# Performance work log

Measured on AMD Instinct MI355X. Metric: run time of the kernel, lower is better.

The kernel has to match this reference:

```python
import jax, jax.numpy as jnp
import numpy as np

B, SX, SY, D = 64, 512, 512, 1024


def setup_inputs() -> dict:
    key = jax.random.key(0)
    k1, k2, k3, k4 = jax.random.split(key, 4)
    x = jax.random.normal(k1, (B, SX, D), dtype=jnp.float32)
    y = jax.random.normal(k2, (B, SY, D), dtype=jnp.float32)
    # Keras 'uniform' init ~ U(-0.05, 0.05); scale kept small and realistic
    W = jax.random.uniform(k3, (D, D), dtype=jnp.float32, minval=-0.05, maxval=0.05)
    b = jax.random.uniform(k4, (D,), dtype=jnp.float32, minval=-0.05, maxval=0.05)
    return {"x": x, "y": y, "W": W, "b": b}


def reference(x, y, W, b):
    # proj: (x @ W + b) -> [B, Sx, D]
    proj = jnp.einsum('bsd,de->bse', x, W) + b
    # attention scores: proj @ y^T -> [B, Sx, Sy]
    att = jnp.einsum('bsd,btd->bst', proj, y)
    # row-wise stable softmax over last axis (matches manual max-subtract softmax)
    nor = jax.nn.softmax(att, axis=-1)
    # weighted sum over y -> [B, Sx, D]
    return jnp.einsum('bst,btd->bsd', nor, y)
```

## Files before the change

### kernel.cpp

```cpp
#include <hip/hip_runtime.h>


typedef float  f32x4  __attribute__((ext_vector_type(4)));
typedef _Float16 f16x8 __attribute__((ext_vector_type(8)));
typedef _Float16 f16x4 __attribute__((ext_vector_type(4)));
typedef __bf16 bf16x8 __attribute__((ext_vector_type(8)));
typedef __bf16 bf16x4 __attribute__((ext_vector_type(4)));

#define MFMA_F16(a, b, c)  __builtin_amdgcn_mfma_f32_16x16x32_f16((a), (b), (c), 0, 0, 0)
#define MFMA_BF16(a, b, c) __builtin_amdgcn_mfma_f32_16x16x32_bf16((a), (b), (c), 0, 0, 0)

#define WAIT_VM0()  do { asm volatile("s_waitcnt vmcnt(0)" ::: "memory"); \
                         __builtin_amdgcn_sched_barrier(0); } while (0)
#define WAIT_LGKM0() do { asm volatile("s_waitcnt lgkmcnt(0)" ::: "memory"); \
                          __builtin_amdgcn_sched_barrier(0); } while (0)

__device__ __forceinline__ void async16(const void* g, void* lds) {
    __builtin_amdgcn_global_load_lds(
        (const __attribute__((address_space(1))) unsigned int*)g,
        (__attribute__((address_space(3))) unsigned int*)lds, 16, 0, 0);
}


__global__ void prep_y_kernel(const float* __restrict__ y, _Float16* __restrict__ yf,
                              _Float16* __restrict__ yT)
{
    __shared__ _Float16 LT[64][72];
    const int tid = threadIdx.x;
    const int b   = blockIdx.x >> 7;
    const int rem = blockIdx.x & 127;
    const int sy0 = (rem >> 4) * 64;
    const int d0  = (rem & 15) * 64;
    const int r0 = tid >> 4;
    const int c4 = (tid & 15) * 4;
    #pragma unroll
    for (int i = 0; i < 4; ++i) {
        const int r = r0 + i * 16;
        const float4 v = *(const float4*)&y[((size_t)b * 512 + sy0 + r) * 1024 + d0 + c4];
        const f16x4 hv = {(_Float16)v.x, (_Float16)v.y, (_Float16)v.z, (_Float16)v.w};
        *(f16x4*)&yf[((size_t)b * 512 + sy0 + r) * 1024 + d0 + c4] = hv;
        #pragma unroll
        for (int cc = 0; cc < 4; ++cc) {
            const int c = (cc + (tid & 3)) & 3;
            LT[c4 + c][r] = hv[c];
        }
    }
    __syncthreads();
    #pragma unroll
    for (int i = 0; i < 4; ++i) {
        const int dr = r0 + i * 16;
        const f16x4 v = *(const f16x4*)&LT[dr][(tid & 15) * 4];
        *(f16x4*)&yT[((size_t)b * 1024 + d0 + dr) * 512 + sy0 + (tid & 15) * 4] = v;
    }
}

__global__ void prep_w_kernel(const float* __restrict__ W, _Float16* __restrict__ WT)
{
    __shared__ _Float16 LT[64][72];
    const int tid = threadIdx.x;
    const int k0 = (blockIdx.x >> 4) * 64;
    const int n0 = (blockIdx.x & 15) * 64;
    const int r0 = tid >> 4;
    const int c4 = (tid & 15) * 4;
    #pragma unroll
    for (int i = 0; i < 4; ++i) {
        const int r = r0 + i * 16;
        const float4 v = *(const float4*)&W[(size_t)(k0 + r) * 1024 + n0 + c4];
        const f16x4 hv = {(_Float16)v.x, (_Float16)v.y, (_Float16)v.z, (_Float16)v.w};
        #pragma unroll
        for (int cc = 0; cc < 4; ++cc) {
            const int c = (cc + (tid & 3)) & 3;
            LT[c4 + c][r] = hv[c];
        }
    }
    __syncthreads();
    #pragma unroll
    for (int i = 0; i < 4; ++i) {
        const int dr = r0 + i * 16;
        const f16x4 v = *(const f16x4*)&LT[dr][(tid & 15) * 4];
        *(f16x4*)&WT[(size_t)(n0 + dr) * 1024 + k0 + (tid & 15) * 4] = v;
    }
}

__global__ void cvt_hl_kernel(const float4* __restrict__ in, f16x4* __restrict__ oh,
                              f16x4* __restrict__ ol, int n4)
{
    int i = blockIdx.x * blockDim.x + threadIdx.x;
    const int stride = gridDim.x * blockDim.x;
    for (; i < n4; i += stride) {
        const float4 v = in[i];
        const _Float16 h0 = (_Float16)v.x, h1 = (_Float16)v.y,
                       h2 = (_Float16)v.z, h3 = (_Float16)v.w;
        oh[i] = (f16x4){h0, h1, h2, h3};
        ol[i] = (f16x4){(_Float16)(v.x - (float)h0), (_Float16)(v.y - (float)h1),
                        (_Float16)(v.z - (float)h2), (_Float16)(v.w - (float)h3)};
    }
}

template <bool PRE>
__global__ __launch_bounds__(256, 3)
void proj_f16_kernel(const _Float16* __restrict__ xh, const _Float16* __restrict__ xl,
                     const _Float16* __restrict__ WT, const float* __restrict__ W,
                     const float* __restrict__ bias, char* __restrict__ outc)
{
    __shared__ _Float16 Xh[128][32];
    __shared__ _Float16 Xl[128][32];
    __shared__ _Float16 Wf[128][32];

    const int tid = threadIdx.x, lane = tid & 63, wave = tid >> 6;
    const int swz = (blockIdx.x & 7) * 256 + (blockIdx.x >> 3);
    const int m0 = (swz >> 3) * 128, n0 = (swz & 7) * 128;
    const int wm = (wave >> 1) * 64, wn = (wave & 1) * 64;
    const int ar = lane & 15;
    const int qs  = ((lane >> 4) ^ ((lane >> 1) & 3)) * 8;
    const int gcS = ((lane & 3) ^ ((lane >> 3) & 3)) * 8;

    f32x4 acc[4][4];
    #pragma unroll
    for (int i = 0; i < 4; ++i)
        #pragma unroll
        for (int j = 0; j < 4; ++j)
            acc[i][j] = (f32x4){0.f, 0.f, 0.f, 0.f};

    const int lrow = lane >> 2;
    const int wkb = tid & 7;
    const int wn4 = (tid >> 3) * 4;

    for (int k0 = 0; k0 < 1024; k0 += 32) {
        __syncthreads();
        #pragma unroll
        for (int t = 0; t < 2; ++t) {
            const int r = wave * 32 + t * 16 + lrow;
            async16(&xh[(size_t)(m0 + r) * 1024 + k0 + gcS], &Xh[wave * 32 + t * 16][0]);
            async16(&xl[(size_t)(m0 + r) * 1024 + k0 + gcS], &Xl[wave * 32 + t * 16][0]);
            if constexpr (PRE)
                async16(&WT[(size_t)(n0 + r) * 1024 + k0 + gcS], &Wf[wave * 32 + t * 16][0]);
        }
        if constexpr (!PRE) {
            const size_t wb = (size_t)(k0 + wkb * 4) * 1024 + n0 + wn4;
            const float4 v0 = *(const float4*)&W[wb];
            const float4 v1 = *(const float4*)&W[wb + 1024];
            const float4 v2 = *(const float4*)&W[wb + 2048];
            const float4 v3 = *(const float4*)&W[wb + 3072];
            const float rv[4][4] = {{v0.x, v0.y, v0.z, v0.w},
                                    {v1.x, v1.y, v1.z, v1.w},
                                    {v2.x, v2.y, v2.z, v2.w},
                                    {v3.x, v3.y, v3.z, v3.w}};
            #pragma unroll
            for (int j = 0; j < 4; ++j) {
                const int R = wn4 + j;
                const f16x4 hv = {(_Float16)rv[0][j], (_Float16)rv[1][j],
                                  (_Float16)rv[2][j], (_Float16)rv[3][j]};
                const int c = (wkb >> 1) ^ ((R >> 1) & 3);
                *(f16x4*)&Wf[R][c * 8 + (wkb & 1) * 4] = hv;
            }
        }
        __syncthreads();

        f16x8 ah[4], al[4], bf[4];
        #pragma unroll
        for (int f = 0; f < 4; ++f) {
            ah[f] = *(const f16x8*)&Xh[wm + f * 16 + ar][qs];
            al[f] = *(const f16x8*)&Xl[wm + f * 16 + ar][qs];
            bf[f] = *(const f16x8*)&Wf[wn + f * 16 + ar][qs];
        }
        #pragma unroll
        for (int i = 0; i < 4; ++i)
            #pragma unroll
            for (int j = 0; j < 4; ++j) {
                acc[i][j] = MFMA_F16(ah[i], bf[j], acc[i][j]);
                acc[i][j] = MFMA_F16(al[i], bf[j], acc[i][j]);
            }
    }

    const int q4 = (lane >> 4) * 4;
    #pragma unroll
    for (int j = 0; j < 4; ++j) {
        const int n = n0 + wn + j * 16 + ar;
        const float bv = bias[n];
        #pragma unroll
        for (int i = 0; i < 4; ++i)
            #pragma unroll
            for (int r = 0; r < 4; ++r) {
                const int R = m0 + wm + i * 16 + q4 + r;
                const float v = acc[i][j][r] + bv;
                const _Float16 h = (_Float16)v;
                const _Float16 l = (_Float16)(v - (float)h);
                _Float16* rowp = (_Float16*)(outc + (size_t)R * 4096);
                rowp[n] = h;
                rowp[1024 + n] = l;
            }
    }
}

__global__ __launch_bounds__(256, 2)
void attn_f16_kernel(const _Float16* __restrict__ yf, const _Float16* __restrict__ yT,
                     char* __restrict__ outc)
{
    __shared__ __align__(16) char smem[76800];
    _Float16 (*Yst)[32]   = (_Float16(*)[32])smem;
    _Float16 (*Pbuf)[520] = (_Float16(*)[520])smem;
    _Float16 (*Yt)[32]    = (_Float16(*)[32])(smem + 66560);
    float*    Red         = (float*)(smem + 74752);

    const int tid = threadIdx.x, lane = tid & 63, wave = tid >> 6;
    const int swz = (blockIdx.x & 7) * 64 + (blockIdx.x >> 3);
    const int b = swz >> 3, sx0 = (swz & 7) * 64;
    const int pbase = b * 512 + sx0;
    const int ar = lane & 15, q = lane >> 4, qk = q * 8;
    const int qs  = (q ^ ((lane >> 1) & 3)) * 8;
    const int gcS = ((lane & 3) ^ ((lane >> 3) & 3)) * 8;
    const int lrow = lane >> 2;
    const size_t ybase = (size_t)b * 512 * 1024;

    f32x4 s2[4][8];
    #pragma unroll
    for (int ri = 0; ri < 4; ++ri)
        #pragma unroll
        for (int t = 0; t < 8; ++t)
            s2[ri][t] = (f32x4){0.f, 0.f, 0.f, 0.f};

    const char* aptr = outc + (size_t)(pbase + ar) * 4096;

    #pragma unroll
    for (int t = 0; t < 8; ++t) {
        const int r = wave * 128 + t * 16 + lrow;
        async16(&yf[ybase + (size_t)r * 1024 + gcS], &Yst[wave * 128 + t * 16][0]);
    }
    f16x8 aH[4], aL[4];
    #pragma unroll
    for (int ri = 0; ri < 4; ++ri) {
        aH[ri] = *(const f16x8*)(aptr + (size_t)ri * 65536 + (size_t)qk * 2);
        aL[ri] = *(const f16x8*)(aptr + (size_t)ri * 65536 + 2048 + (size_t)qk * 2);
    }

    for (int kk = 0; kk < 32; ++kk) {
        WAIT_VM0();
        f16x8 bf0[8];
        #pragma unroll
        for (int t = 0; t < 8; ++t)
            bf0[t] = *(const f16x8*)&Yst[wave * 128 + t * 16 + ar][qs];
        WAIT_LGKM0();
        if (kk < 31) {
            const int k1 = (kk + 1) * 32;
            #pragma unroll
            for (int t = 0; t < 8; ++t) {
                const int r = wave * 128 + t * 16 + lrow;
                async16(&yf[ybase + (size_t)r * 1024 + k1 + gcS],
                        &Yst[wave * 128 + t * 16][0]);
            }
        }
        #pragma unroll
        for (int ri = 0; ri < 4; ++ri)
            #pragma unroll
            for (int t = 0; t < 8; ++t) {
                s2[ri][t] = MFMA_F16(aH[ri], bf0[t], s2[ri][t]);
                s2[ri][t] = MFMA_F16(aL[ri], bf0[t], s2[ri][t]);
            }
        if (kk < 31) {
            const int k1 = (kk + 1) * 32;
            #pragma unroll
            for (int ri = 0; ri < 4; ++ri) {
                aH[ri] = *(const f16x8*)(aptr + (size_t)ri * 65536 + (size_t)(k1 + qk) * 2);
                aL[ri] = *(const f16x8*)(aptr + (size_t)ri * 65536 + 2048
                                         + (size_t)(k1 + qk) * 2);
            }
        }
    }

    float pm[4][4];
    #pragma unroll
    for (int ri = 0; ri < 4; ++ri)
        #pragma unroll
        for (int r = 0; r < 4; ++r) {
            float m = -3.0e38f;
            #pragma unroll
            for (int t = 0; t < 8; ++t) m = fmaxf(m, s2[ri][t][r]);
            pm[ri][r] = m;
        }
    #pragma unroll
    for (int off = 1; off < 16; off <<= 1)
        #pragma unroll
        for (int ri = 0; ri < 4; ++ri)
            #pragma unroll
            for (int r = 0; r < 4; ++r)
                pm[ri][r] = fmaxf(pm[ri][r], __shfl_xor(pm[ri][r], off, 64));
    if (ar == 0) {
        #pragma unroll
        for (int ri = 0; ri < 4; ++ri)
            #pragma unroll
            for (int r = 0; r < 4; ++r)
                Red[wave * 64 + ri * 16 + q * 4 + r] = pm[ri][r];
    }
    __syncthreads();
    float gm[4][4];
    #pragma unroll
    for (int ri = 0; ri < 4; ++ri)
        #pragma unroll
        for (int r = 0; r < 4; ++r) {
            const int row = ri * 16 + q * 4 + r;
            gm[ri][r] = fmaxf(fmaxf(Red[row], Red[64 + row]),
                              fmaxf(Red[128 + row], Red[192 + row]));
        }
    float ps[4][4];
    #pragma unroll
    for (int ri = 0; ri < 4; ++ri)
        #pragma unroll
        for (int r = 0; r < 4; ++r) {
            float sum = 0.f;
            #pragma unroll
            for (int t = 0; t < 8; ++t) {
                const float e = __expf(s2[ri][t][r] - gm[ri][r]);
                s2[ri][t][r] = e;
                sum += e;
            }
            ps[ri][r] = sum;
        }
    #pragma unroll
    for (int off = 1; off < 16; off <<= 1)
        #pragma unroll
        for (int ri = 0; ri < 4; ++ri)
            #pragma unroll
            for (int r = 0; r < 4; ++r)
                ps[ri][r] += __shfl_xor(ps[ri][r], off, 64);
    if (ar == 0) {
        #pragma unroll
        for (int ri = 0; ri < 4; ++ri)
            #pragma unroll
            for (int r = 0; r < 4; ++r)
                Red[256 + wave * 64 + ri * 16 + q * 4 + r] = ps[ri][r];
    }
    __syncthreads();
    float inv[4][4];
    #pragma unroll
    for (int ri = 0; ri < 4; ++ri)
        #pragma unroll
        for (int r = 0; r < 4; ++r) {
            const int row = 256 + ri * 16 + q * 4 + r;
            inv[ri][r] = 1.0f / (Red[row] + Red[64 + row] + Red[128 + row] + Red[192 + row]);
        }
    #pragma unroll
    for (int ri = 0; ri < 4; ++ri)
        #pragma unroll
        for (int t = 0; t < 8; ++t)
            #pragma unroll
            for (int r = 0; r < 4; ++r)
                Pbuf[ri * 16 + q * 4 + r][wave * 128 + t * 16 + ar]
                    = (_Float16)(s2[ri][t][r] * inv[ri][r]);
    __syncthreads();

    float* outF = (float*)outc;
    for (int dc = 0; dc < 8; ++dc) {
        f32x4 o2[4][2];
        #pragma unroll
        for (int ri = 0; ri < 4; ++ri)
            #pragma unroll
            for (int t = 0; t < 2; ++t)
                o2[ri][t] = (f32x4){0.f, 0.f, 0.f, 0.f};

        WAIT_LGKM0();
        #pragma unroll
        for (int t = 0; t < 2; ++t) {
            const int r = wave * 32 + t * 16 + lrow;
            async16(&yT[(size_t)(b * 1024 + dc * 128 + r) * 512 + gcS],
                    &Yt[wave * 32 + t * 16][0]);
        }
        for (int kk = 0; kk < 16; ++kk) {
            WAIT_VM0();
            f16x8 a2[4], b2[2];
            #pragma unroll
            for (int ri = 0; ri < 4; ++ri)
                a2[ri] = *(const f16x8*)&Pbuf[ri * 16 + ar][kk * 32 + qk];
            #pragma unroll
            for (int t = 0; t < 2; ++t)
                b2[t] = *(const f16x8*)&Yt[wave * 32 + t * 16 + ar][qs];
            WAIT_LGKM0();
            if (kk < 15) {
                const int k1 = (kk + 1) * 32;
                #pragma unroll
                for (int t = 0; t < 2; ++t) {
                    const int r = wave * 32 + t * 16 + lrow;
                    async16(&yT[(size_t)(b * 1024 + dc * 128 + r) * 512 + k1 + gcS],
                            &Yt[wave * 32 + t * 16][0]);
                }
            }
            #pragma unroll
            for (int ri = 0; ri < 4; ++ri)
                #pragma unroll
                for (int t = 0; t < 2; ++t)
                    o2[ri][t] = MFMA_F16(a2[ri], b2[t], o2[ri][t]);
        }
        #pragma unroll
        for (int ri = 0; ri < 4; ++ri)
            #pragma unroll
            for (int t = 0; t < 2; ++t)
                #pragma unroll
                for (int r = 0; r < 4; ++r)
                    outF[(size_t)(pbase + ri * 16 + q * 4 + r) * 1024
                         + dc * 128 + wave * 32 + t * 16 + ar] = o2[ri][t][r];
    }
}


__device__ __forceinline__ void cvt4(const float4 v, bf16x4& h, bf16x4& l) {
    const float f0 = v.x, f1 = v.y, f2 = v.z, f3 = v.w;
    const __bf16 h0 = (__bf16)f0, h1 = (__bf16)f1, h2 = (__bf16)f2, h3 = (__bf16)f3;
    h = (bf16x4){h0, h1, h2, h3};
    l = (bf16x4){(__bf16)(f0 - (float)h0), (__bf16)(f1 - (float)h1),
                 (__bf16)(f2 - (float)h2), (__bf16)(f3 - (float)h3)};
}

__global__ __launch_bounds__(256, 2)
void proj_kernel_fb(const float* __restrict__ x, const float* __restrict__ W,
                    const float* __restrict__ bias, float* __restrict__ proj)
{
    __shared__ __bf16 Ah[128][40];
    __shared__ __bf16 Al[128][40];
    __shared__ __bf16 Bh[128][40];
    __shared__ __bf16 Bl[128][40];

    const int tid = threadIdx.x, lane = tid & 63, wave = tid >> 6;
    const int wm = (wave >> 1) * 64, wn = (wave & 1) * 64;
    const int m0 = (blockIdx.x >> 3) * 128, n0 = (blockIdx.x & 7) * 128;
    const int ar = lane & 15, ak = (lane >> 4) * 8;

    f32x4 acc[4][4];
    #pragma unroll
    for (int i = 0; i < 4; ++i)
        #pragma unroll
        for (int j = 0; j < 4; ++j)
            acc[i][j] = (f32x4){0.f, 0.f, 0.f, 0.f};

    const int xr = tid >> 3, xc = (tid & 7) * 4;
    const int wkb = tid >> 5, wn4 = (tid & 31) * 4;

    for (int k0 = 0; k0 < 1024; k0 += 32) {
        __syncthreads();
        #pragma unroll
        for (int it = 0; it < 4; ++it) {
            const int r = xr + it * 32;
            const float4 v = *(const float4*)&x[(size_t)(m0 + r) * 1024 + k0 + xc];
            bf16x4 h, l; cvt4(v, h, l);
            *(bf16x4*)&Ah[r][xc] = h;
            *(bf16x4*)&Al[r][xc] = l;
        }
        {
            const size_t wb = (size_t)(k0 + wkb * 4) * 1024 + n0 + wn4;
            const float4 v0 = *(const float4*)&W[wb];
            const float4 v1 = *(const float4*)&W[wb + 1024];
            const float4 v2 = *(const float4*)&W[wb + 2048];
            const float4 v3 = *(const float4*)&W[wb + 3072];
            const float rv[4][4] = {{v0.x, v0.y, v0.z, v0.w},
                                    {v1.x, v1.y, v1.z, v1.w},
                                    {v2.x, v2.y, v2.z, v2.w},
                                    {v3.x, v3.y, v3.z, v3.w}};
            #pragma unroll
            for (int j = 0; j < 4; ++j) {
                bf16x4 h, l;
                #pragma unroll
                for (int kk = 0; kk < 4; ++kk) {
                    const float f = rv[kk][j];
                    const __bf16 hb = (__bf16)f;
                    h[kk] = hb;
                    l[kk] = (__bf16)(f - (float)hb);
                }
                *(bf16x4*)&Bh[wn4 + j][wkb * 4] = h;
                *(bf16x4*)&Bl[wn4 + j][wkb * 4] = l;
            }
        }
        __syncthreads();

        bf16x8 a_h[4], a_l[4], b_h[4], b_l[4];
        #pragma unroll
        for (int f = 0; f < 4; ++f) {
            a_h[f] = *(const bf16x8*)&Ah[wm + f * 16 + ar][ak];
            a_l[f] = *(const bf16x8*)&Al[wm + f * 16 + ar][ak];
            b_h[f] = *(const bf16x8*)&Bh[wn + f * 16 + ar][ak];
            b_l[f] = *(const bf16x8*)&Bl[wn + f * 16 + ar][ak];
        }
        #pragma unroll
        for (int i = 0; i < 4; ++i)
            #pragma unroll
            for (int j = 0; j < 4; ++j) {
                acc[i][j] = MFMA_BF16(a_h[i], b_h[j], acc[i][j]);
                acc[i][j] = MFMA_BF16(a_l[i], b_h[j], acc[i][j]);
                acc[i][j] = MFMA_BF16(a_h[i], b_l[j], acc[i][j]);
            }
    }

    const int q4 = (lane >> 4) * 4;
    #pragma unroll
    for (int j = 0; j < 4; ++j) {
        const int n = n0 + wn + j * 16 + ar;
        const float bv = bias[n];
        #pragma unroll
        for (int i = 0; i < 4; ++i) {
            const size_t base = (size_t)(m0 + wm + i * 16 + q4) * 1024 + n;
            #pragma unroll
            for (int r = 0; r < 4; ++r)
                proj[base + (size_t)r * 1024] = acc[i][j][r] + bv;
        }
    }
}

__global__ __launch_bounds__(256, 1)
void attn_kernel_fb(const float* __restrict__ y, float* __restrict__ out)
{
    __shared__ __bf16 Ph[64][40];
    __shared__ __bf16 Pl[64][40];
    __shared__ __bf16 Yh[128][40];
    __shared__ __bf16 Yl[128][40];
    __shared__ __bf16 Pbuf[64][520];

    const int tid = threadIdx.x, lane = tid & 63, wave = tid >> 6;
    const int b = blockIdx.x >> 3, sx0 = (blockIdx.x & 7) * 64;
    const size_t ybase = (size_t)b * 512 * 1024;
    const size_t pbase = ((size_t)b * 512 + sx0) * 1024;
    const int ar = lane & 15, ak = (lane >> 4) * 8, q = lane >> 4;

    f32x4 s[4][8];
    #pragma unroll
    for (int nb = 0; nb < 4; ++nb)
        #pragma unroll
        for (int f = 0; f < 8; ++f)
            s[nb][f] = (f32x4){0.f, 0.f, 0.f, 0.f};

    const int pr = tid >> 3, pc = (tid & 7) * 4;

    for (int k0 = 0; k0 < 1024; k0 += 32) {
        __syncthreads();
        #pragma unroll
        for (int it = 0; it < 2; ++it) {
            const int r = pr + it * 32;
            const float4 v = *(const float4*)&out[pbase + (size_t)r * 1024 + k0 + pc];
            bf16x4 h, l; cvt4(v, h, l);
            *(bf16x4*)&Ph[r][pc] = h;
            *(bf16x4*)&Pl[r][pc] = l;
        }
        #pragma unroll
        for (int nb = 0; nb < 4; ++nb) {
            if (nb) __syncthreads();
            const int sy0 = nb * 128;
            #pragma unroll
            for (int it = 0; it < 4; ++it) {
                const int r = pr + it * 32;
                const float4 v = *(const float4*)&y[ybase + (size_t)(sy0 + r) * 1024 + k0 + pc];
                bf16x4 h, l; cvt4(v, h, l);
                *(bf16x4*)&Yh[r][pc] = h;
                *(bf16x4*)&Yl[r][pc] = l;
            }
            __syncthreads();
            const bf16x8 a_h = *(const bf16x8*)&Ph[wave * 16 + ar][ak];
            const bf16x8 a_l = *(const bf16x8*)&Pl[wave * 16 + ar][ak];
            #pragma unroll
            for (int f = 0; f < 8; ++f) {
                const bf16x8 b_h = *(const bf16x8*)&Yh[f * 16 + ar][ak];
                const bf16x8 b_l = *(const bf16x8*)&Yl[f * 16 + ar][ak];
                s[nb][f] = MFMA_BF16(a_h, b_h, s[nb][f]);
                s[nb][f] = MFMA_BF16(a_l, b_h, s[nb][f]);
                s[nb][f] = MFMA_BF16(a_h, b_l, s[nb][f]);
            }
        }
    }

    #pragma unroll
    for (int r = 0; r < 4; ++r) {
        float m = -3.0e38f;
        #pragma unroll
        for (int nb = 0; nb < 4; ++nb)
            #pragma unroll
            for (int f = 0; f < 8; ++f)
                m = fmaxf(m, s[nb][f][r]);
        #pragma unroll
        for (int off = 1; off < 16; off <<= 1)
            m = fmaxf(m, __shfl_xor(m, off, 64));
        float sum = 0.f;
        #pragma unroll
        for (int nb = 0; nb < 4; ++nb)
            #pragma unroll
            for (int f = 0; f < 8; ++f) {
                const float e = __expf(s[nb][f][r] - m);
                s[nb][f][r] = e;
                sum += e;
            }
        #pragma unroll
        for (int off = 1; off < 16; off <<= 1)
            sum += __shfl_xor(sum, off, 64);
        const float inv = 1.0f / sum;
        #pragma unroll
        for (int nb = 0; nb < 4; ++nb)
            #pragma unroll
            for (int f = 0; f < 8; ++f)
                s[nb][f][r] *= inv;
    }
    #pragma unroll
    for (int nb = 0; nb < 4; ++nb)
        #pragma unroll
        for (int f = 0; f < 8; ++f)
            #pragma unroll
            for (int r = 0; r < 4; ++r)
                Pbuf[wave * 16 + q * 4 + r][nb * 128 + f * 16 + ar] = (__bf16)s[nb][f][r];

    const int y2kb = tid >> 5, y2n4 = (tid & 31) * 4;
    for (int d0 = 0; d0 < 1024; d0 += 128) {
        f32x4 o[8];
        #pragma unroll
        for (int f = 0; f < 8; ++f) o[f] = (f32x4){0.f, 0.f, 0.f, 0.f};

        for (int k0 = 0; k0 < 512; k0 += 32) {
            __syncthreads();
            const size_t yb = ybase + (size_t)(k0 + y2kb * 4) * 1024 + d0 + y2n4;
            const float4 v0 = *(const float4*)&y[yb];
            const float4 v1 = *(const float4*)&y[yb + 1024];
            const float4 v2 = *(const float4*)&y[yb + 2048];
            const float4 v3 = *(const float4*)&y[yb + 3072];
            const float rv[4][4] = {{v0.x, v0.y, v0.z, v0.w},
                                    {v1.x, v1.y, v1.z, v1.w},
                                    {v2.x, v2.y, v2.z, v2.w},
                                    {v3.x, v3.y, v3.z, v3.w}};
            #pragma unroll
            for (int j = 0; j < 4; ++j) {
                const bf16x4 h = (bf16x4){(__bf16)rv[0][j], (__bf16)rv[1][j],
                                          (__bf16)rv[2][j], (__bf16)rv[3][j]};
                *(bf16x4*)&Yh[y2n4 + j][y2kb * 4] = h;
            }
            __syncthreads();
            const bf16x8 a = *(const bf16x8*)&Pbuf[wave * 16 + ar][k0 + ak];
            #pragma unroll
            for (int f = 0; f < 8; ++f) {
                const bf16x8 bb = *(const bf16x8*)&Yh[f * 16 + ar][ak];
                o[f] = MFMA_BF16(a, bb, o[f]);
            }
        }
        #pragma unroll
        for (int f = 0; f < 8; ++f)
            #pragma unroll
            for (int r = 0; r < 4; ++r)
                out[pbase + (size_t)(wave * 16 + q * 4 + r) * 1024 + d0 + f * 16 + ar] = o[f][r];
    }
}


extern "C" void kernel_launch(void* const* d_in, const int* in_sizes, int n_in,
                              void* d_out, int out_size, void* d_ws, size_t ws_size,
                              hipStream_t stream) {
    (void)in_sizes; (void)n_in; (void)out_size;
    const float* x    = (const float*)d_in[0];
    const float* y    = (const float*)d_in[1];
    const float* W    = (const float*)d_in[2];
    const float* bias = (const float*)d_in[3];

    if (ws_size >= 268435456ULL) {
        _Float16* yf = (_Float16*)d_ws;
        _Float16* yT = yf + 33554432;
        _Float16* xh = yT + 33554432;
        _Float16* xl = xh + 33554432;
        _Float16* WT = xl + 33554432;
        const bool pre = ws_size >= 268435456ULL + 2097152ULL;

        prep_y_kernel<<<dim3(8192), dim3(256), 0, stream>>>(y, yf, yT);
        cvt_hl_kernel<<<dim3(2048), dim3(256), 0, stream>>>((const float4*)x, (f16x4*)xh,
                                                            (f16x4*)xl, 8388608);
        if (pre) {
            prep_w_kernel<<<dim3(256), dim3(256), 0, stream>>>(W, WT);
            proj_f16_kernel<true><<<dim3(2048), dim3(256), 0, stream>>>(xh, xl, WT, W, bias,
                                                                        (char*)d_out);
        } else {
            proj_f16_kernel<false><<<dim3(2048), dim3(256), 0, stream>>>(xh, xl, nullptr, W,
                                                                         bias, (char*)d_out);
        }
        attn_f16_kernel<<<dim3(512), dim3(256), 0, stream>>>(yf, yT, (char*)d_out);
    } else {
        float* out = (float*)d_out;
        proj_kernel_fb<<<dim3(256 * 8), dim3(256), 0, stream>>>(x, W, bias, out);
        attn_kernel_fb<<<dim3(64 * 8), dim3(256), 0, stream>>>(y, out);
    }
}
```

Before: 703.4 us.

## Double-buffer proj and attention loads, interleave proj hi/lo layout, swizzle P buffer

The projection GEMM gets double-buffered LDS stages with one barrier per k-step instead of two. The proj output's hi/lo halves are interleaved in 8-element groups so the attention kernel can read both from one contiguous 32-byte chunk. The attention kernel prefetches A fragments two steps ahead into registers, splits the Y staging into halves so loads overlap MFMA, and uses partial vmcnt waits. The softmax P buffer gets an XOR-swizzled layout and the second GEMM uses two rotating Yt buffers with a prefetch distance of two. Together these target load latency and LDS bank conflicts, at the cost of higher register and LDS pressure (AH/AL arrays and 80KB smem) that could reduce occupancy.

```diff
diff --git a/kernel.cpp b/kernel.cpp
--- a/kernel.cpp
+++ b/kernel.cpp
@@ -10,10 +10,11 @@
 #define MFMA_F16(a, b, c)  __builtin_amdgcn_mfma_f32_16x16x32_f16((a), (b), (c), 0, 0, 0)
 #define MFMA_BF16(a, b, c) __builtin_amdgcn_mfma_f32_16x16x32_bf16((a), (b), (c), 0, 0, 0)
 
-#define WAIT_VM0()  do { asm volatile("s_waitcnt vmcnt(0)" ::: "memory"); \
+#define WAIT_VM(N)  do { asm volatile("s_waitcnt vmcnt(" #N ")" ::: "memory"); \
                          __builtin_amdgcn_sched_barrier(0); } while (0)
 #define WAIT_LGKM0() do { asm volatile("s_waitcnt lgkmcnt(0)" ::: "memory"); \
                           __builtin_amdgcn_sched_barrier(0); } while (0)
+#define SB0() __builtin_amdgcn_sched_barrier(0)
 
 __device__ __forceinline__ void async16(const void* g, void* lds) {
     __builtin_amdgcn_global_load_lds(
@@ -103,9 +104,9 @@
                      const _Float16* __restrict__ WT, const float* __restrict__ W,
                      const float* __restrict__ bias, char* __restrict__ outc)
 {
-    __shared__ _Float16 Xh[128][32];
-    __shared__ _Float16 Xl[128][32];
-    __shared__ _Float16 Wf[128][32];
+    __shared__ _Float16 Xh[2][128][32];
+    __shared__ _Float16 Xl[2][128][32];
+    __shared__ _Float16 Wf[2][128][32];
 
     const int tid = threadIdx.x, lane = tid & 63, wave = tid >> 6;
     const int swz = (blockIdx.x & 7) * 256 + (blockIdx.x >> 3);
@@ -114,27 +115,26 @@
     const int ar = lane & 15;
     const int qs  = ((lane >> 4) ^ ((lane >> 1) & 3)) * 8;
     const int gcS = ((lane & 3) ^ ((lane >> 3) & 3)) * 8;
-
-    f32x4 acc[4][4];
-    #pragma unroll
-    for (int i = 0; i < 4; ++i)
-        #pragma unroll
-        for (int j = 0; j < 4; ++j)
-            acc[i][j] = (f32x4){0.f, 0.f, 0.f, 0.f};
-
     const int lrow = lane >> 2;
     const int wkb = tid & 7;
     const int wn4 = (tid >> 3) * 4;
 
-    for (int k0 = 0; k0 < 1024; k0 += 32) {
-        __syncthreads();
-        #pragma unroll
-        for (int t = 0; t < 2; ++t) {
-            const int r = wave * 32 + t * 16 + lrow;
-            async16(&xh[(size_t)(m0 + r) * 1024 + k0 + gcS], &Xh[wave * 32 + t * 16][0]);
-            async16(&xl[(size_t)(m0 + r) * 1024 + k0 + gcS], &Xl[wave * 32 + t * 16][0]);
+    f32x4 acc[4][4];
+    #pragma unroll
+    for (int i = 0; i < 4; ++i)
+        #pragma unroll
+        for (int j = 0; j < 4; ++j)
+            acc[i][j] = (f32x4){0.f, 0.f, 0.f, 0.f};
+
+    auto STAGE = [&](int t, int bi) {
+        const int k0 = t * 32;
+        #pragma unroll
+        for (int tt = 0; tt < 2; ++tt) {
+            const int r = wave * 32 + tt * 16 + lrow;
+            async16(&xh[(size_t)(m0 + r) * 1024 + k0 + gcS], &Xh[bi][wave * 32 + tt * 16][0]);
+            async16(&xl[(size_t)(m0 + r) * 1024 + k0 + gcS], &Xl[bi][wave * 32 + tt * 16][0]);
             if constexpr (PRE)
-                async16(&WT[(size_t)(n0 + r) * 1024 + k0 + gcS], &Wf[wave * 32 + t * 16][0]);
+                async16(&WT[(size_t)(n0 + r) * 1024 + k0 + gcS], &Wf[bi][wave * 32 + tt * 16][0]);
         }
         if constexpr (!PRE) {
             const size_t wb = (size_t)(k0 + wkb * 4) * 1024 + n0 + wn4;
@@ -152,17 +152,23 @@
                 const f16x4 hv = {(_Float16)rv[0][j], (_Float16)rv[1][j],
                                   (_Float16)rv[2][j], (_Float16)rv[3][j]};
                 const int c = (wkb >> 1) ^ ((R >> 1) & 3);
-                *(f16x4*)&Wf[R][c * 8 + (wkb & 1) * 4] = hv;
-            }
-        }
-        __syncthreads();
-
+                *(f16x4*)&Wf[bi][R][c * 8 + (wkb & 1) * 4] = hv;
+            }
+        }
+    };
+
+    STAGE(0, 0);
+    __syncthreads();
+
+    for (int t = 0; t < 32; ++t) {
+        const int cur = t & 1;
+        if (t < 31) STAGE(t + 1, cur ^ 1);
         f16x8 ah[4], al[4], bf[4];
         #pragma unroll
         for (int f = 0; f < 4; ++f) {
-            ah[f] = *(const f16x8*)&Xh[wm + f * 16 + ar][qs];
-            al[f] = *(const f16x8*)&Xl[wm + f * 16 + ar][qs];
-            bf[f] = *(const f16x8*)&Wf[wn + f * 16 + ar][qs];
+            ah[f] = *(const f16x8*)&Xh[cur][wm + f * 16 + ar][qs];
+            al[f] = *(const f16x8*)&Xl[cur][wm + f * 16 + ar][qs];
+            bf[f] = *(const f16x8*)&Wf[cur][wn + f * 16 + ar][qs];
         }
         #pragma unroll
         for (int i = 0; i < 4; ++i)
@@ -171,6 +177,7 @@
                 acc[i][j] = MFMA_F16(ah[i], bf[j], acc[i][j]);
                 acc[i][j] = MFMA_F16(al[i], bf[j], acc[i][j]);
             }
+        __syncthreads();
     }
 
     const int q4 = (lane >> 4) * 4;
@@ -178,6 +185,7 @@
     for (int j = 0; j < 4; ++j) {
         const int n = n0 + wn + j * 16 + ar;
         const float bv = bias[n];
+        const int hidx = (n >> 3) * 16 + (n & 7);
         #pragma unroll
         for (int i = 0; i < 4; ++i)
             #pragma unroll
@@ -187,8 +195,8 @@
                 const _Float16 h = (_Float16)v;
                 const _Float16 l = (_Float16)(v - (float)h);
                 _Float16* rowp = (_Float16*)(outc + (size_t)R * 4096);
-                rowp[n] = h;
-                rowp[1024 + n] = l;
+                rowp[hidx] = h;
+                rowp[hidx + 8] = l;
             }
     }
 }
@@ -197,17 +205,18 @@
 void attn_f16_kernel(const _Float16* __restrict__ yf, const _Float16* __restrict__ yT,
                      char* __restrict__ outc)
 {
-    __shared__ __align__(16) char smem[76800];
-    _Float16 (*Yst)[32]   = (_Float16(*)[32])smem;
-    _Float16 (*Pbuf)[520] = (_Float16(*)[520])smem;
-    _Float16 (*Yt)[32]    = (_Float16(*)[32])(smem + 66560);
-    float*    Red         = (float*)(smem + 74752);
+    __shared__ __align__(16) char smem[81920];
+    _Float16 (*Yst)[32] = (_Float16(*)[32])smem;
+    _Float16* Pb        = (_Float16*)smem;
+    _Float16 (*Yt0)[32] = (_Float16(*)[32])(smem + 65536);
+    _Float16 (*Yt1)[32] = (_Float16(*)[32])(smem + 73728);
+    float*    Red       = (float*)(smem + 73728);
 
     const int tid = threadIdx.x, lane = tid & 63, wave = tid >> 6;
-    const int swz = (blockIdx.x & 7) * 64 + (blockIdx.x >> 3);
-    const int b = swz >> 3, sx0 = (swz & 7) * 64;
+    const int swzb = (blockIdx.x & 7) * 64 + (blockIdx.x >> 3);
+    const int b = swzb >> 3, sx0 = (swzb & 7) * 64;
     const int pbase = b * 512 + sx0;
-    const int ar = lane & 15, q = lane >> 4, qk = q * 8;
+    const int ar = lane & 15, q = lane >> 4;
     const int qs  = (q ^ ((lane >> 1) & 3)) * 8;
     const int gcS = ((lane & 3) ^ ((lane >> 3) & 3)) * 8;
     const int lrow = lane >> 2;
@@ -222,50 +231,73 @@
 
     const char* aptr = outc + (size_t)(pbase + ar) * 4096;
 
+    f16x8 AH[34][4], AL[34][4];
+
     #pragma unroll
     for (int t = 0; t < 8; ++t) {
         const int r = wave * 128 + t * 16 + lrow;
         async16(&yf[ybase + (size_t)r * 1024 + gcS], &Yst[wave * 128 + t * 16][0]);
     }
-    f16x8 aH[4], aL[4];
-    #pragma unroll
-    for (int ri = 0; ri < 4; ++ri) {
-        aH[ri] = *(const f16x8*)(aptr + (size_t)ri * 65536 + (size_t)qk * 2);
-        aL[ri] = *(const f16x8*)(aptr + (size_t)ri * 65536 + 2048 + (size_t)qk * 2);
-    }
-
+    #pragma unroll
+    for (int kk = 0; kk < 2; ++kk)
+        #pragma unroll
+        for (int ri = 0; ri < 4; ++ri) {
+            AH[kk][ri] = *(const f16x8*)(aptr + (size_t)ri * 65536 + (kk * 4 + q) * 32);
+            AL[kk][ri] = *(const f16x8*)(aptr + (size_t)ri * 65536 + (kk * 4 + q) * 32 + 16);
+        }
+
+    #pragma unroll
     for (int kk = 0; kk < 32; ++kk) {
-        WAIT_VM0();
-        f16x8 bf0[8];
-        #pragma unroll
-        for (int t = 0; t < 8; ++t)
-            bf0[t] = *(const f16x8*)&Yst[wave * 128 + t * 16 + ar][qs];
+        if (kk < 31) { WAIT_VM(8); } else { WAIT_VM(0); }
+        f16x8 bfA[4];
+        #pragma unroll
+        for (int t = 0; t < 4; ++t)
+            bfA[t] = *(const f16x8*)&Yst[wave * 128 + t * 16 + ar][qs];
         WAIT_LGKM0();
         if (kk < 31) {
             const int k1 = (kk + 1) * 32;
             #pragma unroll
-            for (int t = 0; t < 8; ++t) {
+            for (int t = 0; t < 4; ++t) {
                 const int r = wave * 128 + t * 16 + lrow;
-                async16(&yf[ybase + (size_t)r * 1024 + k1 + gcS],
-                        &Yst[wave * 128 + t * 16][0]);
-            }
-        }
+                async16(&yf[ybase + (size_t)r * 1024 + k1 + gcS], &Yst[wave * 128 + t * 16][0]);
+            }
+        }
+        if (kk < 30) {
+            #pragma unroll
+            for (int ri = 0; ri < 4; ++ri) {
+                AH[kk + 2][ri] = *(const f16x8*)(aptr + (size_t)ri * 65536 + ((kk + 2) * 4 + q) * 32);
+                AL[kk + 2][ri] = *(const f16x8*)(aptr + (size_t)ri * 65536 + ((kk + 2) * 4 + q) * 32 + 16);
+            }
+        }
+        SB0();
         #pragma unroll
         for (int ri = 0; ri < 4; ++ri)
             #pragma unroll
-            for (int t = 0; t < 8; ++t) {
-                s2[ri][t] = MFMA_F16(aH[ri], bf0[t], s2[ri][t]);
-                s2[ri][t] = MFMA_F16(aL[ri], bf0[t], s2[ri][t]);
-            }
+            for (int t = 0; t < 4; ++t) {
+                s2[ri][t] = MFMA_F16(AH[kk][ri], bfA[t], s2[ri][t]);
+                s2[ri][t] = MFMA_F16(AL[kk][ri], bfA[t], s2[ri][t]);
+            }
+        f16x8 bfB[4];
+        #pragma unroll
+        for (int t = 4; t < 8; ++t)
+            bfB[t - 4] = *(const f16x8*)&Yst[wave * 128 + t * 16 + ar][qs];
+        WAIT_LGKM0();
         if (kk < 31) {
             const int k1 = (kk + 1) * 32;
             #pragma unroll
-            for (int ri = 0; ri < 4; ++ri) {
-                aH[ri] = *(const f16x8*)(aptr + (size_t)ri * 65536 + (size_t)(k1 + qk) * 2);
-                aL[ri] = *(const f16x8*)(aptr + (size_t)ri * 65536 + 2048
-                                         + (size_t)(k1 + qk) * 2);
-            }
-        }
+            for (int t = 4; t < 8; ++t) {
+                const int r = wave * 128 + t * 16 + lrow;
+                async16(&yf[ybase + (size_t)r * 1024 + k1 + gcS], &Yst[wave * 128 + t * 16][0]);
+            }
+        }
+        SB0();
+        #pragma unroll
+        for (int ri = 0; ri < 4; ++ri)
+            #pragma unroll
+            for (int t = 4; t < 8; ++t) {
+                s2[ri][t] = MFMA_F16(AH[kk][ri], bfB[t - 4], s2[ri][t]);
+                s2[ri][t] = MFMA_F16(AL[kk][ri], bfB[t - 4], s2[ri][t]);
+            }
     }
 
     float pm[4][4];
@@ -344,12 +376,28 @@
         #pragma unroll
         for (int t = 0; t < 8; ++t)
             #pragma unroll
-            for (int r = 0; r < 4; ++r)
-                Pbuf[ri * 16 + q * 4 + r][wave * 128 + t * 16 + ar]
+            for (int r = 0; r < 4; ++r) {
+                const int row = ri * 16 + q * 4 + r;
+                const int c = wave * 16 + t * 2 + (ar >> 3);
+                Pb[row * 512 + ((c ^ (row & 7)) << 3) + (ar & 7)]
                     = (_Float16)(s2[ri][t][r] * inv[ri][r]);
+            }
     __syncthreads();
 
     float* outF = (float*)outc;
+    #pragma unroll
+    for (int t = 0; t < 2; ++t) {
+        const int r = wave * 32 + t * 16 + lrow;
+        async16(&yT[(size_t)(b * 1024 + 0 * 128 + r) * 512 + 0 * 32 + gcS],
+                &Yt0[wave * 32 + t * 16][0]);
+    }
+    #pragma unroll
+    for (int t = 0; t < 2; ++t) {
+        const int r = wave * 32 + t * 16 + lrow;
+        async16(&yT[(size_t)(b * 1024 + 0 * 128 + r) * 512 + 1 * 32 + gcS],
+                &Yt1[wave * 32 + t * 16][0]);
+    }
+
     for (int dc = 0; dc < 8; ++dc) {
         f32x4 o2[4][2];
         #pragma unroll
@@ -358,32 +406,39 @@
             for (int t = 0; t < 2; ++t)
                 o2[ri][t] = (f32x4){0.f, 0.f, 0.f, 0.f};
 
-        WAIT_LGKM0();
-        #pragma unroll
-        for (int t = 0; t < 2; ++t) {
-            const int r = wave * 32 + t * 16 + lrow;
-            async16(&yT[(size_t)(b * 1024 + dc * 128 + r) * 512 + gcS],
-                    &Yt[wave * 32 + t * 16][0]);
-        }
+        #pragma unroll
         for (int kk = 0; kk < 16; ++kk) {
-            WAIT_VM0();
+            if (kk == 0) {
+                if (dc == 0) { WAIT_VM(2); } else { WAIT_VM(10); }
+            } else if (kk == 15) {
+                if (dc == 7) { WAIT_VM(0); } else { WAIT_VM(2); }
+            } else {
+                WAIT_VM(2);
+            }
+            _Float16 (*Ycur)[32] = (kk & 1) ? Yt1 : Yt0;
             f16x8 a2[4], b2[2];
             #pragma unroll
-            for (int ri = 0; ri < 4; ++ri)
-                a2[ri] = *(const f16x8*)&Pbuf[ri * 16 + ar][kk * 32 + qk];
+            for (int ri = 0; ri < 4; ++ri) {
+                const int rowa = ri * 16 + ar;
+                a2[ri] = *(const f16x8*)&Pb[rowa * 512 + (((kk * 4 + q) ^ (ar & 7)) << 3)];
+            }
             #pragma unroll
             for (int t = 0; t < 2; ++t)
-                b2[t] = *(const f16x8*)&Yt[wave * 32 + t * 16 + ar][qs];
+                b2[t] = *(const f16x8*)&Ycur[wave * 32 + t * 16 + ar][qs];
             WAIT_LGKM0();
-            if (kk < 15) {
-                const int k1 = (kk + 1) * 32;
-                #pragma unroll
-                for (int t = 0; t < 2; ++t) {
-                    const int r = wave * 32 + t * 16 + lrow;
-                    async16(&yT[(size_t)(b * 1024 + dc * 128 + r) * 512 + k1 + gcS],
-                            &Yt[wave * 32 + t * 16][0]);
+            {
+                const int kk2 = (kk + 2) & 15;
+                const int dc2 = dc + ((kk + 2) >> 4);
+                if (dc2 < 8) {
+                    #pragma unroll
+                    for (int t = 0; t < 2; ++t) {
+                        const int r = wave * 32 + t * 16 + lrow;
+                        async16(&yT[(size_t)(b * 1024 + dc2 * 128 + r) * 512 + kk2 * 32 + gcS],
+                                &Ycur[wave * 32 + t * 16][0]);
+                    }
                 }
             }
+            SB0();
             #pragma unroll
             for (int ri = 0; ri < 4; ++ri)
                 #pragma unroll
```

Result: slower. 812.5 us (+15.5%).

## Double-buffer proj GEMM, interleave hi/lo proj layout, read y directly from global in attention

Applied to the files above, without the earlier changes.

The projection GEMM now double-buffers its LDS tiles so the next K-slice loads while MFMAs run, with one barrier per iteration. Its output interleaves the fp16 hi/lo halves in 8-element groups, so the attention kernel fetches each pair with one contiguous load. The attention kernel drops LDS staging of y and yT and reads B fragments straight from global memory, keeping two A fragments in registers as a prefetch. The PV stage is restructured so each wave computes 128 output columns per pass with more accumulators, which raises register pressure and relies on caches for the repeated global reads.

```diff
diff --git a/kernel.cpp b/kernel.cpp
--- a/kernel.cpp
+++ b/kernel.cpp
@@ -9,11 +9,6 @@
 
 #define MFMA_F16(a, b, c)  __builtin_amdgcn_mfma_f32_16x16x32_f16((a), (b), (c), 0, 0, 0)
 #define MFMA_BF16(a, b, c) __builtin_amdgcn_mfma_f32_16x16x32_bf16((a), (b), (c), 0, 0, 0)
-
-#define WAIT_VM0()  do { asm volatile("s_waitcnt vmcnt(0)" ::: "memory"); \
-                         __builtin_amdgcn_sched_barrier(0); } while (0)
-#define WAIT_LGKM0() do { asm volatile("s_waitcnt lgkmcnt(0)" ::: "memory"); \
-                          __builtin_amdgcn_sched_barrier(0); } while (0)
 
 __device__ __forceinline__ void async16(const void* g, void* lds) {
     __builtin_amdgcn_global_load_lds(
@@ -103,9 +98,9 @@
                      const _Float16* __restrict__ WT, const float* __restrict__ W,
                      const float* __restrict__ bias, char* __restrict__ outc)
 {
-    __shared__ _Float16 Xh[128][32];
-    __shared__ _Float16 Xl[128][32];
-    __shared__ _Float16 Wf[128][32];
+    __shared__ _Float16 Xh[2][128][32];
+    __shared__ _Float16 Xl[2][128][32];
+    __shared__ _Float16 Wf[2][128][32];
 
     const int tid = threadIdx.x, lane = tid & 63, wave = tid >> 6;
     const int swz = (blockIdx.x & 7) * 256 + (blockIdx.x >> 3);
@@ -114,27 +109,26 @@
     const int ar = lane & 15;
     const int qs  = ((lane >> 4) ^ ((lane >> 1) & 3)) * 8;
     const int gcS = ((lane & 3) ^ ((lane >> 3) & 3)) * 8;
-
-    f32x4 acc[4][4];
-    #pragma unroll
-    for (int i = 0; i < 4; ++i)
-        #pragma unroll
-        for (int j = 0; j < 4; ++j)
-            acc[i][j] = (f32x4){0.f, 0.f, 0.f, 0.f};
-
     const int lrow = lane >> 2;
     const int wkb = tid & 7;
     const int wn4 = (tid >> 3) * 4;
 
-    for (int k0 = 0; k0 < 1024; k0 += 32) {
-        __syncthreads();
-        #pragma unroll
-        for (int t = 0; t < 2; ++t) {
-            const int r = wave * 32 + t * 16 + lrow;
-            async16(&xh[(size_t)(m0 + r) * 1024 + k0 + gcS], &Xh[wave * 32 + t * 16][0]);
-            async16(&xl[(size_t)(m0 + r) * 1024 + k0 + gcS], &Xl[wave * 32 + t * 16][0]);
+    f32x4 acc[4][4];
+    #pragma unroll
+    for (int i = 0; i < 4; ++i)
+        #pragma unroll
+        for (int j = 0; j < 4; ++j)
+            acc[i][j] = (f32x4){0.f, 0.f, 0.f, 0.f};
+
+    auto STAGE = [&](int t, int bi) {
+        const int k0 = t * 32;
+        #pragma unroll
+        for (int tt = 0; tt < 2; ++tt) {
+            const int r = wave * 32 + tt * 16 + lrow;
+            async16(&xh[(size_t)(m0 + r) * 1024 + k0 + gcS], &Xh[bi][wave * 32 + tt * 16][0]);
+            async16(&xl[(size_t)(m0 + r) * 1024 + k0 + gcS], &Xl[bi][wave * 32 + tt * 16][0]);
             if constexpr (PRE)
-                async16(&WT[(size_t)(n0 + r) * 1024 + k0 + gcS], &Wf[wave * 32 + t * 16][0]);
+                async16(&WT[(size_t)(n0 + r) * 1024 + k0 + gcS], &Wf[bi][wave * 32 + tt * 16][0]);
         }
         if constexpr (!PRE) {
             const size_t wb = (size_t)(k0 + wkb * 4) * 1024 + n0 + wn4;
@@ -152,17 +146,23 @@
                 const f16x4 hv = {(_Float16)rv[0][j], (_Float16)rv[1][j],
                                   (_Float16)rv[2][j], (_Float16)rv[3][j]};
                 const int c = (wkb >> 1) ^ ((R >> 1) & 3);
-                *(f16x4*)&Wf[R][c * 8 + (wkb & 1) * 4] = hv;
-            }
-        }
-        __syncthreads();
-
+                *(f16x4*)&Wf[bi][R][c * 8 + (wkb & 1) * 4] = hv;
+            }
+        }
+    };
+
+    STAGE(0, 0);
+    __syncthreads();
+
+    for (int t = 0; t < 32; ++t) {
+        const int cur = t & 1;
+        if (t < 31) STAGE(t + 1, cur ^ 1);
         f16x8 ah[4], al[4], bf[4];
         #pragma unroll
         for (int f = 0; f < 4; ++f) {
-            ah[f] = *(const f16x8*)&Xh[wm + f * 16 + ar][qs];
-            al[f] = *(const f16x8*)&Xl[wm + f * 16 + ar][qs];
-            bf[f] = *(const f16x8*)&Wf[wn + f * 16 + ar][qs];
+            ah[f] = *(const f16x8*)&Xh[cur][wm + f * 16 + ar][qs];
+            al[f] = *(const f16x8*)&Xl[cur][wm + f * 16 + ar][qs];
+            bf[f] = *(const f16x8*)&Wf[cur][wn + f * 16 + ar][qs];
         }
         #pragma unroll
         for (int i = 0; i < 4; ++i)
@@ -171,6 +171,7 @@
                 acc[i][j] = MFMA_F16(ah[i], bf[j], acc[i][j]);
                 acc[i][j] = MFMA_F16(al[i], bf[j], acc[i][j]);
             }
+        __syncthreads();
     }
 
     const int q4 = (lane >> 4) * 4;
@@ -178,6 +179,7 @@
     for (int j = 0; j < 4; ++j) {
         const int n = n0 + wn + j * 16 + ar;
         const float bv = bias[n];
+        const int hidx = (n >> 3) * 16 + (n & 7);
         #pragma unroll
         for (int i = 0; i < 4; ++i)
             #pragma unroll
@@ -187,8 +189,8 @@
                 const _Float16 h = (_Float16)v;
                 const _Float16 l = (_Float16)(v - (float)h);
                 _Float16* rowp = (_Float16*)(outc + (size_t)R * 4096);
-                rowp[n] = h;
-                rowp[1024 + n] = l;
+                rowp[hidx] = h;
+                rowp[hidx + 8] = l;
             }
     }
 }
@@ -197,20 +199,14 @@
 void attn_f16_kernel(const _Float16* __restrict__ yf, const _Float16* __restrict__ yT,
                      char* __restrict__ outc)
 {
-    __shared__ __align__(16) char smem[76800];
-    _Float16 (*Yst)[32]   = (_Float16(*)[32])smem;
-    _Float16 (*Pbuf)[520] = (_Float16(*)[520])smem;
-    _Float16 (*Yt)[32]    = (_Float16(*)[32])(smem + 66560);
-    float*    Red         = (float*)(smem + 74752);
+    __shared__ _Float16 Pbuf[64][520];
+    __shared__ float    Red[512];
 
     const int tid = threadIdx.x, lane = tid & 63, wave = tid >> 6;
-    const int swz = (blockIdx.x & 7) * 64 + (blockIdx.x >> 3);
-    const int b = swz >> 3, sx0 = (swz & 7) * 64;
+    const int swzb = (blockIdx.x & 7) * 64 + (blockIdx.x >> 3);
+    const int b = swzb >> 3, sx0 = (swzb & 7) * 64;
     const int pbase = b * 512 + sx0;
     const int ar = lane & 15, q = lane >> 4, qk = q * 8;
-    const int qs  = (q ^ ((lane >> 1) & 3)) * 8;
-    const int gcS = ((lane & 3) ^ ((lane >> 3) & 3)) * 8;
-    const int lrow = lane >> 2;
     const size_t ybase = (size_t)b * 512 * 1024;
 
     f32x4 s2[4][8];
@@ -221,50 +217,49 @@
             s2[ri][t] = (f32x4){0.f, 0.f, 0.f, 0.f};
 
     const char* aptr = outc + (size_t)(pbase + ar) * 4096;
-
-    #pragma unroll
-    for (int t = 0; t < 8; ++t) {
-        const int r = wave * 128 + t * 16 + lrow;
-        async16(&yf[ybase + (size_t)r * 1024 + gcS], &Yst[wave * 128 + t * 16][0]);
-    }
-    f16x8 aH[4], aL[4];
-    #pragma unroll
-    for (int ri = 0; ri < 4; ++ri) {
-        aH[ri] = *(const f16x8*)(aptr + (size_t)ri * 65536 + (size_t)qk * 2);
-        aL[ri] = *(const f16x8*)(aptr + (size_t)ri * 65536 + 2048 + (size_t)qk * 2);
-    }
-
-    for (int kk = 0; kk < 32; ++kk) {
-        WAIT_VM0();
-        f16x8 bf0[8];
-        #pragma unroll
-        for (int t = 0; t < 8; ++t)
-            bf0[t] = *(const f16x8*)&Yst[wave * 128 + t * 16 + ar][qs];
-        WAIT_LGKM0();
-        if (kk < 31) {
-            const int k1 = (kk + 1) * 32;
-            #pragma unroll
-            for (int t = 0; t < 8; ++t) {
-                const int r = wave * 128 + t * 16 + lrow;
-                async16(&yf[ybase + (size_t)r * 1024 + k1 + gcS],
-                        &Yst[wave * 128 + t * 16][0]);
-            }
-        }
-        #pragma unroll
-        for (int ri = 0; ri < 4; ++ri)
-            #pragma unroll
-            for (int t = 0; t < 8; ++t) {
-                s2[ri][t] = MFMA_F16(aH[ri], bf0[t], s2[ri][t]);
-                s2[ri][t] = MFMA_F16(aL[ri], bf0[t], s2[ri][t]);
-            }
-        if (kk < 31) {
-            const int k1 = (kk + 1) * 32;
-            #pragma unroll
-            for (int ri = 0; ri < 4; ++ri) {
-                aH[ri] = *(const f16x8*)(aptr + (size_t)ri * 65536 + (size_t)(k1 + qk) * 2);
-                aL[ri] = *(const f16x8*)(aptr + (size_t)ri * 65536 + 2048
-                                         + (size_t)(k1 + qk) * 2);
-            }
+    const _Float16* yw = yf + ybase + (size_t)(wave * 128 + ar) * 1024;
+
+    f16x8 A0H[4], A0L[4], A1H[4], A1L[4];
+    auto LOADA = [&](int kk, f16x8 (&AH)[4], f16x8 (&AL)[4]) {
+        #pragma unroll
+        for (int ri = 0; ri < 4; ++ri) {
+            const char* p = aptr + (size_t)ri * 65536 + (size_t)(kk * 4 + q) * 32;
+            AH[ri] = *(const f16x8*)p;
+            AL[ri] = *(const f16x8*)(p + 16);
+        }
+    };
+
+    LOADA(0, A0H, A0L);
+    LOADA(1, A1H, A1L);
+
+    for (int kk = 0; kk < 32; kk += 2) {
+        {
+            f16x8 bf[8];
+            #pragma unroll
+            for (int t = 0; t < 8; ++t)
+                bf[t] = *(const f16x8*)&yw[(size_t)t * 16384 + kk * 32 + qk];
+            #pragma unroll
+            for (int ri = 0; ri < 4; ++ri)
+                #pragma unroll
+                for (int t = 0; t < 8; ++t) {
+                    s2[ri][t] = MFMA_F16(A0H[ri], bf[t], s2[ri][t]);
+                    s2[ri][t] = MFMA_F16(A0L[ri], bf[t], s2[ri][t]);
+                }
+            if (kk + 2 < 32) LOADA(kk + 2, A0H, A0L);
+        }
+        {
+            f16x8 bf[8];
+            #pragma unroll
+            for (int t = 0; t < 8; ++t)
+                bf[t] = *(const f16x8*)&yw[(size_t)t * 16384 + (kk + 1) * 32 + qk];
+            #pragma unroll
+            for (int ri = 0; ri < 4; ++ri)
+                #pragma unroll
+                for (int t = 0; t < 8; ++t) {
+                    s2[ri][t] = MFMA_F16(A1H[ri], bf[t], s2[ri][t]);
+                    s2[ri][t] = MFMA_F16(A1L[ri], bf[t], s2[ri][t]);
+                }
+            if (kk + 3 < 32) LOADA(kk + 3, A1H, A1L);
         }
     }
 
@@ -350,54 +345,39 @@
     __syncthreads();
 
     float* outF = (float*)outc;
-    for (int dc = 0; dc < 8; ++dc) {
-        f32x4 o2[4][2];
+    #pragma unroll
+    for (int dc = 0; dc < 2; ++dc) {
+        f32x4 o2[4][8];
         #pragma unroll
         for (int ri = 0; ri < 4; ++ri)
             #pragma unroll
-            for (int t = 0; t < 2; ++t)
+            for (int t = 0; t < 8; ++t)
                 o2[ri][t] = (f32x4){0.f, 0.f, 0.f, 0.f};
 
-        WAIT_LGKM0();
-        #pragma unroll
-        for (int t = 0; t < 2; ++t) {
-            const int r = wave * 32 + t * 16 + lrow;
-            async16(&yT[(size_t)(b * 1024 + dc * 128 + r) * 512 + gcS],
-                    &Yt[wave * 32 + t * 16][0]);
-        }
+        const _Float16* ytw = yT + ((size_t)b * 1024 + wave * 256 + dc * 128 + ar) * 512;
+
         for (int kk = 0; kk < 16; ++kk) {
-            WAIT_VM0();
-            f16x8 a2[4], b2[2];
+            f16x8 a2[4], b2[8];
             #pragma unroll
             for (int ri = 0; ri < 4; ++ri)
                 a2[ri] = *(const f16x8*)&Pbuf[ri * 16 + ar][kk * 32 + qk];
             #pragma unroll
-            for (int t = 0; t < 2; ++t)
-                b2[t] = *(const f16x8*)&Yt[wave * 32 + t * 16 + ar][qs];
-            WAIT_LGKM0();
-            if (kk < 15) {
-                const int k1 = (kk + 1) * 32;
-                #pragma unroll
-                for (int t = 0; t < 2; ++t) {
-                    const int r = wave * 32 + t * 16 + lrow;
-                    async16(&yT[(size_t)(b * 1024 + dc * 128 + r) * 512 + k1 + gcS],
-                            &Yt[wave * 32 + t * 16][0]);
-                }
-            }
+            for (int t = 0; t < 8; ++t)
+                b2[t] = *(const f16x8*)&ytw[(size_t)t * 16 * 512 + kk * 32 + qk];
             #pragma unroll
             for (int ri = 0; ri < 4; ++ri)
                 #pragma unroll
-                for (int t = 0; t < 2; ++t)
+                for (int t = 0; t < 8; ++t)
                     o2[ri][t] = MFMA_F16(a2[ri], b2[t], o2[ri][t]);
         }
         #pragma unroll
         for (int ri = 0; ri < 4; ++ri)
             #pragma unroll
-            for (int t = 0; t < 2; ++t)
+            for (int t = 0; t < 8; ++t)
                 #pragma unroll
                 for (int r = 0; r < 4; ++r)
                     outF[(size_t)(pbase + ri * 16 + q * 4 + r) * 1024
-                         + dc * 128 + wave * 32 + t * 16 + ar] = o2[ri][t][r];
+                         + wave * 256 + dc * 128 + t * 16 + ar] = o2[ri][t][r];
     }
 }
 
```

After: 707.2 us. About the same (+0.5%).
